# Performance work log

Measured on AMD Instinct MI355X. Metric: run time of the kernel, lower is better.

Reference implementation:

```python
import jax, jax.numpy as jnp
import numpy as np

N = 4096        # num_nodes
IN = 256        # in_channels
HEADS = 8
F = 64          # out_channels per head
E = 131072      # num_edges (avg degree 32)
NEG_SLOPE = 0.2


def setup_inputs() -> dict:
    key = jax.random.key(0)
    k1, k2, k3, k4 = jax.random.split(key, 4)
    x = jax.random.normal(k1, (N, IN), dtype=jnp.float32)
    edge_index = jax.random.randint(k2, (2, E), 0, N, dtype=jnp.int64)
    # Linear(in, heads*out, bias=False): stored as [IN, HEADS*F] so h = x @ W
    W = jax.random.normal(k3, (IN, HEADS * F), dtype=jnp.float32) * (1.0 / np.sqrt(IN))
    a = jax.random.normal(k4, (HEADS, 2 * F), dtype=jnp.float32) * 0.1
    return {"x": x, "edge_index": edge_index, "W": W, "a": a}


def reference(x, edge_index, W, a):
    n = x.shape[0]
    h = (x @ W).reshape(n, HEADS, F)  # [N, H, F]

    # Dense adjacency with self loops (faithful to original: adj[src,dst]=1 + eye)
    adj = jnp.zeros((n, n), dtype=x.dtype).at[edge_index[0], edge_index[1]].set(1.0)
    adj = adj + jnp.eye(n, dtype=x.dtype)
    masked = adj == 0  # [N, N]

    # e[i,j,h] = leaky_relu([h_i, h_j] . a_h) = leaky_relu(h_i.a1_h + h_j.a2_h)
    a_src, a_dst = a[:, :F], a[:, F:]
    e_src = jnp.einsum('nhf,hf->nh', h, a_src)  # contribution of row node i
    e_dst = jnp.einsum('nhf,hf->nh', h, a_dst)  # contribution of col node j
    e = jax.nn.leaky_relu(e_src[:, None, :] + e_dst[None, :, :], NEG_SLOPE)  # [N,N,H]
    e = jnp.where(masked[:, :, None], -jnp.inf, e)

    # softmax over neighbors j (dim=1 in original); dropout is identity in eval mode
    alpha = jax.nn.softmax(e, axis=1)  # [N, N, H]

    out = jnp.einsum('ijh,jhf->ihf', alpha, h)  # [N, H, F]
    return out.reshape(n, HEADS * F)  # concat=True
```

## Files before the change

kernel.cpp:

```cpp
#include <hip/hip_runtime.h>

#define NNODES 4096
#define INF_   256
#define HEADS  8
#define FDIM   64
#define HO     512
#define NEDGES 131072
#define NEG_SLOPE 0.2f
#define MWORDS 128

#define ZB 512
#define XB 1024
#define WB 512
#define GEMM_BLOCKS 512
#define ADJ_BLOCKS  512
#define LCAP 1092

typedef unsigned short ushort_t;
typedef short bf16x8 __attribute__((ext_vector_type(8)));
typedef float f32x4  __attribute__((ext_vector_type(4)));

union U16x8 { uint4 u; bf16x8 v; };

__device__ __forceinline__ float bf16_to_f32(ushort_t u) {
    union { unsigned int i; float f; } c;
    c.i = ((unsigned int)u) << 16;
    return c.f;
}
__device__ __forceinline__ ushort_t f32_to_bf16(float f) {
    union { float f; unsigned int i; } c;
    c.f = f;
    unsigned int r = c.i + 0x7FFF + ((c.i >> 16) & 1);
    return (ushort_t)(r >> 16);
}

__global__ __launch_bounds__(256) void prep_kernel(const float* __restrict__ x,
                                                   const float* __restrict__ W,
                                                   unsigned int* __restrict__ mask,
                                                   ushort_t* __restrict__ xb,
                                                   ushort_t* __restrict__ wt) {
    int b = blockIdx.x, t = threadIdx.x;
    if (b < ZB) {
        *reinterpret_cast<uint4*>(mask + (size_t)(b * 256 + t) * 4) = make_uint4(0u, 0u, 0u, 0u);
    } else if (b < ZB + XB) {
        int i = (b - ZB) * 256 + t;
        float4 v = *reinterpret_cast<const float4*>(x + (size_t)i * 4);
        ushort4 o;
        o.x = f32_to_bf16(v.x); o.y = f32_to_bf16(v.y);
        o.z = f32_to_bf16(v.z); o.w = f32_to_bf16(v.w);
        *reinterpret_cast<ushort4*>(xb + (size_t)i * 4) = o;
    } else {
        int e = (b - ZB - XB) * 256 + t;
        int k = e >> 9, n = e & 511;
        wt[(size_t)n * INF_ + k] = f32_to_bf16(W[e]);
    }
}

__global__ __launch_bounds__(256) void gemm_adj(const ushort_t* __restrict__ xb,
                                                const ushort_t* __restrict__ wt,
                                                const float* __restrict__ a,
                                                const int* __restrict__ ei,
                                                unsigned int* __restrict__ mask,
                                                ushort_t* __restrict__ hout,
                                                float* __restrict__ es,
                                                float* __restrict__ ed) {
    int b = blockIdx.x, t = threadIdx.x;

    if (b >= GEMM_BLOCKS) {
        int e = (b - GEMM_BLOCKS) * 256 + t;
        if (e < NEDGES) {
            int src = ei[e];
            int dst = ei[NEDGES + e];
            atomicOr(&mask[src * MWORDS + (dst >> 5)], 1u << (dst & 31));
        }
        if (e < NNODES) {
            atomicOr(&mask[e * MWORDS + (e >> 5)], 1u << (e & 31));
        }
        return;
    }

    int bi = b >> 3, bj = b & 7;
    int w  = t >> 6, l = t & 63;
    int lr = l & 15, lk = l >> 4;

    const ushort_t* ap = xb + (size_t)(bi * 64 + w * 16 + lr) * INF_ + lk * 8;
    const ushort_t* bp = wt + (size_t)(bj * 64 + lr) * INF_ + lk * 8;

    f32x4 acc[4];
    #pragma unroll
    for (int c = 0; c < 4; ++c) acc[c] = (f32x4){0.f, 0.f, 0.f, 0.f};

    #pragma unroll
    for (int k0 = 0; k0 < INF_; k0 += 32) {
        U16x8 af;
        af.u = *reinterpret_cast<const uint4*>(ap + k0);
        #pragma unroll
        for (int c = 0; c < 4; ++c) {
            U16x8 bf_;
            bf_.u = *reinterpret_cast<const uint4*>(bp + (size_t)c * 16 * INF_ + k0);
            acc[c] = __builtin_amdgcn_mfma_f32_16x16x32_bf16(af.v, bf_.v, acc[c], 0, 0, 0);
        }
    }

    int growbase = bi * 64 + w * 16 + lk * 4;
    #pragma unroll
    for (int c = 0; c < 4; ++c) {
        int gcol = bj * 64 + c * 16 + lr;
        #pragma unroll
        for (int r = 0; r < 4; ++r)
            hout[(size_t)(growbase + r) * HO + gcol] = f32_to_bf16(acc[c][r]);
    }

    float ps[4] = {0.f, 0.f, 0.f, 0.f}, pd[4] = {0.f, 0.f, 0.f, 0.f};
    #pragma unroll
    for (int c = 0; c < 4; ++c) {
        int col64 = c * 16 + lr;
        float as_ = a[bj * 2 * FDIM + col64];
        float ad_ = a[bj * 2 * FDIM + FDIM + col64];
        #pragma unroll
        for (int r = 0; r < 4; ++r) {
            ps[r] += acc[c][r] * as_;
            pd[r] += acc[c][r] * ad_;
        }
    }
    #pragma unroll
    for (int r = 0; r < 4; ++r) {
        #pragma unroll
        for (int off = 1; off < 16; off <<= 1) {
            ps[r] += __shfl_xor(ps[r], off, 16);
            pd[r] += __shfl_xor(pd[r], off, 16);
        }
        if (lr == 0) {
            int grow = growbase + r;
            es[grow * HEADS + bj] = ps[r];
            ed[grow * HEADS + bj] = pd[r];
        }
    }
}

__global__ __launch_bounds__(256) void gat_aggregate(const ushort_t* __restrict__ h,
                                                     const float* __restrict__ es,
                                                     const float* __restrict__ ed,
                                                     const unsigned int* __restrict__ mask,
                                                     float* __restrict__ out) {
    int w = threadIdx.x >> 6, lane = threadIdx.x & 63;
    int i = blockIdx.x * 4 + w;
    __shared__ unsigned short list_s[4][LCAP];
    unsigned short* mylist = list_s[w];

    const unsigned int* row = mask + (size_t)i * MWORDS;
    unsigned int b0 = row[lane], b1 = row[64 + lane];
    int c0 = __popc(b0), c1 = __popc(b1);
    int s0 = c0;
    #pragma unroll
    for (int off = 1; off < 64; off <<= 1) { int v = __shfl_up(s0, off); if (lane >= off) s0 += v; }
    int tot0 = __shfl(s0, 63);
    int s1 = c1;
    #pragma unroll
    for (int off = 1; off < 64; off <<= 1) { int v = __shfl_up(s1, off); if (lane >= off) s1 += v; }
    int deg = tot0 + __shfl(s1, 63);
    int p0 = s0 - c0;
    int p1 = tot0 + s1 - c1;
    int base0 = lane * 32, base1 = (64 + lane) * 32;
    while (b0) {
        int bit = __ffs(b0) - 1; b0 &= b0 - 1;
        if (p0 < LCAP) mylist[p0] = (unsigned short)(base0 + bit);
        ++p0;
    }
    while (b1) {
        int bit = __ffs(b1) - 1; b1 &= b1 - 1;
        if (p1 < LCAP) mylist[p1] = (unsigned short)(base1 + bit);
        ++p1;
    }
    __syncthreads();

    int hh = lane >> 3;
    int f0 = lane * 8;
    float es_h = es[i * HEADS + hh];
    float acc[8] = {0.f, 0.f, 0.f, 0.f, 0.f, 0.f, 0.f, 0.f};
    float den = 0.f;
    int jj = 0;
    for (; jj + 2 <= deg; jj += 2) {
        int ja = mylist[jj], jb = mylist[jj + 1];
        float ea = ed[ja * HEADS + hh];
        float eb = ed[jb * HEADS + hh];
        uint4 va = *reinterpret_cast<const uint4*>(h + (size_t)ja * HO + f0);
        uint4 vb = *reinterpret_cast<const uint4*>(h + (size_t)jb * HO + f0);
        float sa = es_h + ea; sa = sa > 0.f ? sa : NEG_SLOPE * sa;
        float sb = es_h + eb; sb = sb > 0.f ? sb : NEG_SLOPE * sb;
        float wa = __expf(sa), wb = __expf(sb);
        den += wa + wb;
        acc[0] += wa * bf16_to_f32((ushort_t)(va.x & 0xFFFF)) + wb * bf16_to_f32((ushort_t)(vb.x & 0xFFFF));
        acc[1] += wa * bf16_to_f32((ushort_t)(va.x >> 16))    + wb * bf16_to_f32((ushort_t)(vb.x >> 16));
        acc[2] += wa * bf16_to_f32((ushort_t)(va.y & 0xFFFF)) + wb * bf16_to_f32((ushort_t)(vb.y & 0xFFFF));
        acc[3] += wa * bf16_to_f32((ushort_t)(va.y >> 16))    + wb * bf16_to_f32((ushort_t)(vb.y >> 16));
        acc[4] += wa * bf16_to_f32((ushort_t)(va.z & 0xFFFF)) + wb * bf16_to_f32((ushort_t)(vb.z & 0xFFFF));
        acc[5] += wa * bf16_to_f32((ushort_t)(va.z >> 16))    + wb * bf16_to_f32((ushort_t)(vb.z >> 16));
        acc[6] += wa * bf16_to_f32((ushort_t)(va.w & 0xFFFF)) + wb * bf16_to_f32((ushort_t)(vb.w & 0xFFFF));
        acc[7] += wa * bf16_to_f32((ushort_t)(va.w >> 16))    + wb * bf16_to_f32((ushort_t)(vb.w >> 16));
    }
    if (jj < deg) {
        int ja = mylist[jj];
        float ea = ed[ja * HEADS + hh];
        uint4 va = *reinterpret_cast<const uint4*>(h + (size_t)ja * HO + f0);
        float sa = es_h + ea; sa = sa > 0.f ? sa : NEG_SLOPE * sa;
        float wa = __expf(sa);
        den += wa;
        acc[0] += wa * bf16_to_f32((ushort_t)(va.x & 0xFFFF));
        acc[1] += wa * bf16_to_f32((ushort_t)(va.x >> 16));
        acc[2] += wa * bf16_to_f32((ushort_t)(va.y & 0xFFFF));
        acc[3] += wa * bf16_to_f32((ushort_t)(va.y >> 16));
        acc[4] += wa * bf16_to_f32((ushort_t)(va.z & 0xFFFF));
        acc[5] += wa * bf16_to_f32((ushort_t)(va.z >> 16));
        acc[6] += wa * bf16_to_f32((ushort_t)(va.w & 0xFFFF));
        acc[7] += wa * bf16_to_f32((ushort_t)(va.w >> 16));
    }

    float inv = 1.0f / den;
    float4 o0 = {acc[0] * inv, acc[1] * inv, acc[2] * inv, acc[3] * inv};
    float4 o1 = {acc[4] * inv, acc[5] * inv, acc[6] * inv, acc[7] * inv};
    float* op = out + (size_t)i * HO + f0;
    *reinterpret_cast<float4*>(op) = o0;
    *reinterpret_cast<float4*>(op + 4) = o1;
}

extern "C" void kernel_launch(void* const* d_in, const int* in_sizes, int n_in,
                              void* d_out, int out_size, void* d_ws, size_t ws_size,
                              hipStream_t stream) {
    const float* x  = (const float*)d_in[0];
    const int*   ei = (const int*)d_in[1];
    const float* W  = (const float*)d_in[2];
    const float* a  = (const float*)d_in[3];
    float* out = (float*)d_out;

    char* ws = (char*)d_ws;
    ushort_t* h  = (ushort_t*)ws;
    float* es = (float*)(ws + (size_t)NNODES * HO * 2);
    float* ed = es + NNODES * HEADS;
    unsigned int* mask = (unsigned int*)(ed + NNODES * HEADS);
    ushort_t* xb = (ushort_t*)(mask + (size_t)NNODES * MWORDS);
    ushort_t* wt = xb + (size_t)NNODES * INF_;

    hipLaunchKernelGGL(prep_kernel, dim3(ZB + XB + WB), dim3(256), 0, stream,
                       x, W, mask, xb, wt);
    hipLaunchKernelGGL(gemm_adj, dim3(GEMM_BLOCKS + ADJ_BLOCKS), dim3(256), 0, stream,
                       xb, wt, a, ei, mask, h, es, ed);
    hipLaunchKernelGGL(gat_aggregate, dim3(NNODES / 4), dim3(256), 0, stream, h, es, ed, mask, out);
}
```

Before: 37.96 us.

## Tile W transpose through shared memory, unroll aggregation by four, nontemporal output stores

The W-to-bf16 transpose now goes through a 64x64 shared-memory tile per block, using 32 blocks instead of 512 with strided scalar writes, so both the reads and the writes are coalesced. The aggregation loop over neighbours is unrolled from two to four, which keeps more gathers of h and ed in flight per wave. Output stores become nontemporal. The cost is higher register pressure in the aggregation kernel and a shared-memory allocation in every prep block, including the ones that do not use it.

```diff
diff --git a/kernel.cpp b/kernel.cpp
--- a/kernel.cpp
+++ b/kernel.cpp
@@ -11,7 +11,7 @@
 
 #define ZB 512
 #define XB 1024
-#define WB 512
+#define WTB 32
 #define GEMM_BLOCKS 512
 #define ADJ_BLOCKS  512
 #define LCAP 1092
@@ -39,6 +39,7 @@
                                                    unsigned int* __restrict__ mask,
                                                    ushort_t* __restrict__ xb,
                                                    ushort_t* __restrict__ wt) {
+    __shared__ float tile[64][65];
     int b = blockIdx.x, t = threadIdx.x;
     if (b < ZB) {
         *reinterpret_cast<uint4*>(mask + (size_t)(b * 256 + t) * 4) = make_uint4(0u, 0u, 0u, 0u);
@@ -50,9 +51,31 @@
         o.z = f32_to_bf16(v.z); o.w = f32_to_bf16(v.w);
         *reinterpret_cast<ushort4*>(xb + (size_t)i * 4) = o;
     } else {
-        int e = (b - ZB - XB) * 256 + t;
-        int k = e >> 9, n = e & 511;
-        wt[(size_t)n * INF_ + k] = f32_to_bf16(W[e]);
+        int wb = b - ZB - XB;
+        int k0 = (wb >> 3) * 64;
+        int n0 = (wb & 7) * 64;
+        int row = t >> 2, c4 = t & 3;
+        #pragma unroll
+        for (int it = 0; it < 4; ++it) {
+            int f4 = c4 + it * 4;
+            float4 v = *reinterpret_cast<const float4*>(&W[(size_t)(k0 + row) * HO + n0 + f4 * 4]);
+            tile[row][f4 * 4 + 0] = v.x;
+            tile[row][f4 * 4 + 1] = v.y;
+            tile[row][f4 * 4 + 2] = v.z;
+            tile[row][f4 * 4 + 3] = v.w;
+        }
+        __syncthreads();
+        int n = t >> 2;
+        #pragma unroll
+        for (int it = 0; it < 4; ++it) {
+            int ch = (t & 3) + it * 4;
+            ushort4 o;
+            o.x = f32_to_bf16(tile[ch * 4 + 0][n]);
+            o.y = f32_to_bf16(tile[ch * 4 + 1][n]);
+            o.z = f32_to_bf16(tile[ch * 4 + 2][n]);
+            o.w = f32_to_bf16(tile[ch * 4 + 3][n]);
+            *reinterpret_cast<ushort4*>(&wt[(size_t)(n0 + n) * INF_ + k0 + ch * 4]) = o;
+        }
     }
 }
 
@@ -138,6 +161,17 @@
     }
 }
 
+__device__ __forceinline__ void agg_one(float wgt, uint4 v, float* acc) {
+    acc[0] += wgt * bf16_to_f32((ushort_t)(v.x & 0xFFFF));
+    acc[1] += wgt * bf16_to_f32((ushort_t)(v.x >> 16));
+    acc[2] += wgt * bf16_to_f32((ushort_t)(v.y & 0xFFFF));
+    acc[3] += wgt * bf16_to_f32((ushort_t)(v.y >> 16));
+    acc[4] += wgt * bf16_to_f32((ushort_t)(v.z & 0xFFFF));
+    acc[5] += wgt * bf16_to_f32((ushort_t)(v.z >> 16));
+    acc[6] += wgt * bf16_to_f32((ushort_t)(v.w & 0xFFFF));
+    acc[7] += wgt * bf16_to_f32((ushort_t)(v.w >> 16));
+}
+
 __global__ __launch_bounds__(256) void gat_aggregate(const ushort_t* __restrict__ h,
                                                      const float* __restrict__ es,
                                                      const float* __restrict__ ed,
@@ -180,48 +214,43 @@
     float acc[8] = {0.f, 0.f, 0.f, 0.f, 0.f, 0.f, 0.f, 0.f};
     float den = 0.f;
     int jj = 0;
-    for (; jj + 2 <= deg; jj += 2) {
-        int ja = mylist[jj], jb = mylist[jj + 1];
+    for (; jj + 4 <= deg; jj += 4) {
+        int ja = mylist[jj], jb = mylist[jj + 1], jc = mylist[jj + 2], jd = mylist[jj + 3];
         float ea = ed[ja * HEADS + hh];
         float eb = ed[jb * HEADS + hh];
+        float ec = ed[jc * HEADS + hh];
+        float ee = ed[jd * HEADS + hh];
         uint4 va = *reinterpret_cast<const uint4*>(h + (size_t)ja * HO + f0);
         uint4 vb = *reinterpret_cast<const uint4*>(h + (size_t)jb * HO + f0);
+        uint4 vc = *reinterpret_cast<const uint4*>(h + (size_t)jc * HO + f0);
+        uint4 vd = *reinterpret_cast<const uint4*>(h + (size_t)jd * HO + f0);
         float sa = es_h + ea; sa = sa > 0.f ? sa : NEG_SLOPE * sa;
         float sb = es_h + eb; sb = sb > 0.f ? sb : NEG_SLOPE * sb;
-        float wa = __expf(sa), wb = __expf(sb);
-        den += wa + wb;
-        acc[0] += wa * bf16_to_f32((ushort_t)(va.x & 0xFFFF)) + wb * bf16_to_f32((ushort_t)(vb.x & 0xFFFF));
-        acc[1] += wa * bf16_to_f32((ushort_t)(va.x >> 16))    + wb * bf16_to_f32((ushort_t)(vb.x >> 16));
-        acc[2] += wa * bf16_to_f32((ushort_t)(va.y & 0xFFFF)) + wb * bf16_to_f32((ushort_t)(vb.y & 0xFFFF));
-        acc[3] += wa * bf16_to_f32((ushort_t)(va.y >> 16))    + wb * bf16_to_f32((ushort_t)(vb.y >> 16));
-        acc[4] += wa * bf16_to_f32((ushort_t)(va.z & 0xFFFF)) + wb * bf16_to_f32((ushort_t)(vb.z & 0xFFFF));
-        acc[5] += wa * bf16_to_f32((ushort_t)(va.z >> 16))    + wb * bf16_to_f32((ushort_t)(vb.z >> 16));
-        acc[6] += wa * bf16_to_f32((ushort_t)(va.w & 0xFFFF)) + wb * bf16_to_f32((ushort_t)(vb.w & 0xFFFF));
-        acc[7] += wa * bf16_to_f32((ushort_t)(va.w >> 16))    + wb * bf16_to_f32((ushort_t)(vb.w >> 16));
-    }
-    if (jj < deg) {
+        float sc = es_h + ec; sc = sc > 0.f ? sc : NEG_SLOPE * sc;
+        float sd = es_h + ee; sd = sd > 0.f ? sd : NEG_SLOPE * sd;
+        float wa = __expf(sa), wb = __expf(sb), wc = __expf(sc), wd = __expf(sd);
+        den += (wa + wb) + (wc + wd);
+        agg_one(wa, va, acc);
+        agg_one(wb, vb, acc);
+        agg_one(wc, vc, acc);
+        agg_one(wd, vd, acc);
+    }
+    for (; jj < deg; ++jj) {
         int ja = mylist[jj];
         float ea = ed[ja * HEADS + hh];
         uint4 va = *reinterpret_cast<const uint4*>(h + (size_t)ja * HO + f0);
         float sa = es_h + ea; sa = sa > 0.f ? sa : NEG_SLOPE * sa;
         float wa = __expf(sa);
         den += wa;
-        acc[0] += wa * bf16_to_f32((ushort_t)(va.x & 0xFFFF));
-        acc[1] += wa * bf16_to_f32((ushort_t)(va.x >> 16));
-        acc[2] += wa * bf16_to_f32((ushort_t)(va.y & 0xFFFF));
-        acc[3] += wa * bf16_to_f32((ushort_t)(va.y >> 16));
-        acc[4] += wa * bf16_to_f32((ushort_t)(va.z & 0xFFFF));
-        acc[5] += wa * bf16_to_f32((ushort_t)(va.z >> 16));
-        acc[6] += wa * bf16_to_f32((ushort_t)(va.w & 0xFFFF));
-        acc[7] += wa * bf16_to_f32((ushort_t)(va.w >> 16));
+        agg_one(wa, va, acc);
     }
 
     float inv = 1.0f / den;
-    float4 o0 = {acc[0] * inv, acc[1] * inv, acc[2] * inv, acc[3] * inv};
-    float4 o1 = {acc[4] * inv, acc[5] * inv, acc[6] * inv, acc[7] * inv};
+    f32x4 o0 = {acc[0] * inv, acc[1] * inv, acc[2] * inv, acc[3] * inv};
+    f32x4 o1 = {acc[4] * inv, acc[5] * inv, acc[6] * inv, acc[7] * inv};
     float* op = out + (size_t)i * HO + f0;
-    *reinterpret_cast<float4*>(op) = o0;
-    *reinterpret_cast<float4*>(op + 4) = o1;
+    __builtin_nontemporal_store(o0, reinterpret_cast<f32x4*>(op));
+    __builtin_nontemporal_store(o1, reinterpret_cast<f32x4*>(op + 4));
 }
 
 extern "C" void kernel_launch(void* const* d_in, const int* in_sizes, int n_in,
@@ -241,7 +270,7 @@
     ushort_t* xb = (ushort_t*)(mask + (size_t)NNODES * MWORDS);
     ushort_t* wt = xb + (size_t)NNODES * INF_;
 
-    hipLaunchKernelGGL(prep_kernel, dim3(ZB + XB + WB), dim3(256), 0, stream,
+    hipLaunchKernelGGL(prep_kernel, dim3(ZB + XB + WTB), dim3(256), 0, stream,
                        x, W, mask, xb, wt);
     hipLaunchKernelGGL(gemm_adj, dim3(GEMM_BLOCKS + ADJ_BLOCKS), dim3(256), 0, stream,
                        xb, wt, a, ei, mask, h, es, ed);
```

New measurement: 37.35 us. About the same (-1.6%).
